# Kernel tuning notes

Measured on AMD Instinct MI355X. Metric: run time of the kernel, lower is better.

Reference implementation:

```python
import jax, jax.numpy as jnp
import numpy as np

B, T, C, H = 2, 2048, 1024, 16
HD = C // H

def setup_inputs() -> dict:
    key = jax.random.key(0)
    ks = jax.random.split(key, 5)
    x = jax.random.normal(ks[0], (B, T, C), dtype=jnp.float32)
    # causal mask, broadcast over batch and heads
    mask = jnp.tril(jnp.ones((T, T), dtype=jnp.int32))[None, None]
    scale = 0.02
    qkv_w = jax.random.normal(ks[1], (3 * C, C), dtype=jnp.float32) * scale
    qkv_b = jax.random.normal(ks[2], (3 * C,), dtype=jnp.float32) * scale
    out_w = jax.random.normal(ks[3], (C, C), dtype=jnp.float32) * scale
    out_b = jax.random.normal(ks[4], (C,), dtype=jnp.float32) * scale
    return {"x": x, "mask": mask, "qkv_w": qkv_w, "qkv_b": qkv_b,
            "out_w": out_w, "out_b": out_b}

def reference(x, mask, qkv_w, qkv_b, out_w, out_b):
    b, t, c = x.shape
    # torch Linear: y = x @ W^T + b
    qkv = jnp.einsum('btc,oc->bto', x, qkv_w) + qkv_b  # [B,T,3C]
    q, k, v = jnp.split(qkv, 3, axis=-1)
    def heads(u):
        return u.reshape(b, t, H, HD).transpose(0, 2, 1, 3)  # [B,H,T,HD]
    q, k, v = heads(q), heads(k), heads(v)
    attn = jnp.einsum('bhqd,bhkd->bhqk', q, k) / jnp.sqrt(jnp.float32(HD))
    attn = jnp.where(mask == 0, jnp.float32(-jnp.inf), attn)
    attn = jax.nn.softmax(attn, axis=-1)
    out = jnp.einsum('bhqk,bhkd->bhqd', attn, v)
    out = out.transpose(0, 2, 1, 3).reshape(b, t, c)
    return jnp.einsum('btc,oc->bto', out, out_w) + out_b
```

## Files before the change

kernel.cpp:

```cpp
#include <hip/hip_runtime.h>
#include <hip/hip_bf16.h>
#include <math.h>

#define B_  2
#define T_  2048
#define C_  1024
#define H_  16
#define HD_ 64

typedef __attribute__((ext_vector_type(8))) short short8;
typedef __attribute__((ext_vector_type(4))) float floatx4;

__device__ __forceinline__ short f2bf(float f) {
    __hip_bfloat16 h = __float2bfloat16(f);
    return *reinterpret_cast<short*>(&h);
}

__device__ __forceinline__ float fexp2(float x) {
#if __has_builtin(__builtin_amdgcn_exp2f)
    return __builtin_amdgcn_exp2f(x);
#else
    return exp2f(x);
#endif
}

__device__ __forceinline__ unsigned pack2bf(float a, float b) {
    return __builtin_amdgcn_perm(__float_as_uint(b), __float_as_uint(a),
                                 0x07060302u);
}

__device__ __forceinline__ void gld16(const void* g, void* l) {
    __builtin_amdgcn_global_load_lds(
        (const __attribute__((address_space(1))) void*)g,
        (__attribute__((address_space(3))) void*)l, 16, 0, 0);
}

__global__ __launch_bounds__(256)
void cast3(const float* __restrict__ x, const float* __restrict__ w1,
           const float* __restrict__ w2, short* __restrict__ xo,
           short* __restrict__ w1o, short* __restrict__ w2o)
{
    int gid = blockIdx.x * 256 + threadIdx.x;
    const float* s; short* d; int off;
    if (gid < 524288)      { s = x;  d = xo;  off = gid; }
    else if (gid < 917504) { s = w1; d = w1o; off = gid - 524288; }
    else                   { s = w2; d = w2o; off = gid - 917504; }
    float4 a = ((const float4*)s)[(size_t)off * 2];
    float4 b = ((const float4*)s)[(size_t)off * 2 + 1];
    short8 v;
    v[0] = f2bf(a.x); v[1] = f2bf(a.y); v[2] = f2bf(a.z); v[3] = f2bf(a.w);
    v[4] = f2bf(b.x); v[5] = f2bf(b.y); v[6] = f2bf(b.z); v[7] = f2bf(b.w);
    *(short8*)(d + (size_t)off * 8) = v;
}

template<int MODE, int BM, int BN, int BK>
__global__ __launch_bounds__(256, 4)
void gemm_bf16(const short* __restrict__ A, const short* __restrict__ W,
               const float* __restrict__ bias, float* __restrict__ out,
               short* __restrict__ qb, short* __restrict__ kb,
               short* __restrict__ vt, int M, int N, int K)
{
    constexpr int MI  = BM / 32;
    constexpr int NJ  = BN / 32;
    constexpr int KS  = BK / 32;
    constexpr int CPR = BK / 8;
    constexpr int LC  = (CPR == 8) ? 3 : 4;
    constexpr int RPT = 256 / CPR;
    __shared__ __align__(16) short As[2][BM * BK];
    __shared__ __align__(16) short Bs[2][BN * BK];

    const int tid  = threadIdx.x;
    const int lane = tid & 63;
    const int w    = tid >> 6;
    const int m    = lane & 15, quad = lane >> 4;
    const int wrow = w >> 1, wcol = w & 1;
    const int nb = blockIdx.x, mb = blockIdx.y;

    const int g = (tid & (CPR - 1)) ^ ((tid >> LC) & (CPR - 1));
    const short* Ag = A + (size_t)(mb * BM + (tid >> LC)) * K + g * 8;
    const short* Wg = W + (size_t)(nb * BN + (tid >> LC)) * K + g * 8;

    int aoff[MI][KS], boff[NJ][KS];
#pragma unroll
    for (int i = 0; i < MI; i++) {
        int ar = wrow * (BM / 2) + i * 16 + m;
#pragma unroll
        for (int ks = 0; ks < KS; ks++)
            aoff[i][ks] = ar * BK + (((ks * 4 + quad) ^ (ar & (CPR - 1))) * 8);
    }
#pragma unroll
    for (int j = 0; j < NJ; j++) {
        int bc = wcol * (BN / 2) + j * 16 + m;
#pragma unroll
        for (int ks = 0; ks < KS; ks++)
            boff[j][ks] = bc * BK + (((ks * 4 + quad) ^ (bc & (CPR - 1))) * 8);
    }

    floatx4 acc[MI][NJ];
#pragma unroll
    for (int i = 0; i < MI; i++)
#pragma unroll
        for (int j = 0; j < NJ; j++) acc[i][j] = (floatx4){0.f, 0.f, 0.f, 0.f};

    auto stage = [&](int k0, int bi) {
#pragma unroll
        for (int i = 0; i < BM / RPT; i++)
            gld16(Ag + (size_t)(i * RPT) * K + k0, As[bi] + i * 2048 + tid * 8);
#pragma unroll
        for (int i = 0; i < BN / RPT; i++)
            gld16(Wg + (size_t)(i * RPT) * K + k0, Bs[bi] + i * 2048 + tid * 8);
    };

    const int nk = K / BK;
    stage(0, 0);
    __syncthreads();

    for (int ki = 0; ki < nk; ki++) {
        const int cur = ki & 1;
        if (ki + 1 < nk) stage((ki + 1) * BK, cur ^ 1);

        const short* Ac = &As[cur][0];
        const short* Bc = &Bs[cur][0];
        short8 af[MI][KS], bfr[NJ][KS];
#pragma unroll
        for (int i = 0; i < MI; i++)
#pragma unroll
            for (int ks = 0; ks < KS; ks++)
                af[i][ks] = *(const short8*)(Ac + aoff[i][ks]);
#pragma unroll
        for (int j = 0; j < NJ; j++)
#pragma unroll
            for (int ks = 0; ks < KS; ks++)
                bfr[j][ks] = *(const short8*)(Bc + boff[j][ks]);
#pragma unroll
        for (int i = 0; i < MI; i++)
#pragma unroll
            for (int j = 0; j < NJ; j++)
#pragma unroll
                for (int ks = 0; ks < KS; ks++)
                    acc[i][j] = __builtin_amdgcn_mfma_f32_16x16x32_bf16(
                        af[i][ks], bfr[j][ks], acc[i][j], 0, 0, 0);
        __syncthreads();
    }

    const int row0 = mb * BM + wrow * (BM / 2);
    const int col0 = nb * BN + wcol * (BN / 2);

    if (MODE == 0) {
#pragma unroll
        for (int j = 0; j < NJ; j++) {
            int n = col0 + j * 16 + m;
            float bn = bias[n];
#pragma unroll
            for (int i = 0; i < MI; i++) {
#pragma unroll
                for (int r = 0; r < 4; r++) {
                    int mm = row0 + i * 16 + quad * 4 + r;
                    out[(size_t)mm * N + n] = acc[i][j][r] + bn;
                }
            }
        }
    } else {
        const int sec = col0 >> 10;
        const int h   = (col0 >> 6) & 15;
        if (sec <= 1) {
            short* dst = sec ? kb : qb;
            const float sc = sec ? 1.0f : 0.18033688011112042f;
#pragma unroll
            for (int j = 0; j < NJ; j++) {
                int n = col0 + j * 16 + m;
                int d = n & 63;
                float bn = bias[n];
#pragma unroll
                for (int i = 0; i < MI; i++) {
                    int t0 = row0 + i * 16 + quad * 4;
                    int b  = t0 >> 11;
                    int t  = t0 & (T_ - 1);
#pragma unroll
                    for (int r = 0; r < 4; r++)
                        dst[((size_t)(b * H_ + h) * T_ + t + r) * HD_ + d] =
                            f2bf((acc[i][j][r] + bn) * sc);
                }
            }
        } else {
#pragma unroll
            for (int j = 0; j < NJ; j++) {
                int n = col0 + j * 16 + m;
                int d = n & 63;
                float bn = bias[n];
#pragma unroll
                for (int i = 0; i < MI; i++) {
                    int t0 = row0 + i * 16 + quad * 4;
                    int b  = t0 >> 11;
                    int t  = t0 & (T_ - 1);
                    ushort4 u;
                    u.x = (unsigned short)f2bf(acc[i][j][0] + bn);
                    u.y = (unsigned short)f2bf(acc[i][j][1] + bn);
                    u.z = (unsigned short)f2bf(acc[i][j][2] + bn);
                    u.w = (unsigned short)f2bf(acc[i][j][3] + bn);
                    *(ushort4*)(vt + ((size_t)(b * H_ + h) * HD_ + d) * T_ + t) = u;
                }
            }
        }
    }
}

__global__ __launch_bounds__(256, 4)
void attn_mfma(const short* __restrict__ qb, const short* __restrict__ kb,
               const short* __restrict__ vt, short* __restrict__ ao)
{
    __shared__ __align__(16) short Ks[2][64 * 64];
    __shared__ __align__(16) short Vs[2][64 * 64];
    __shared__ __align__(16) short Ps[4][16 * 64];

    const int tid  = threadIdx.x;
    const int w    = tid >> 6;
    const int lane = tid & 63;
    const int m    = lane & 15;
    const int quad = lane >> 4;

    const int bid = blockIdx.x;
    const int r   = bid >> 8;
    const int bh  = ((bid & 7) << 2) | ((bid >> 3) & 3);
    const int qs  = (bid >> 5) & 7;
    const int qt  = r * 8 + ((r & 1) ? (7 - qs) : qs);
    const int b   = bh >> 4, h = bh & 15;

    int off8[8];
#pragma unroll
    for (int ks = 0; ks < 2; ks++)
#pragma unroll
        for (int nt = 0; nt < 4; nt++)
            off8[ks * 4 + nt] = (nt * 16 + m) * 64 + (((quad + 4 * ks) ^ (m & 7)) * 8);

    short* PsW = &Ps[w][0];
    int pw[4], pr[2];
#pragma unroll
    for (int nt = 0; nt < 4; nt++)
        pw[nt] = m * 64 + (((2 * nt + (quad >> 1)) ^ (m & 7)) * 8) + (quad & 1) * 4;
#pragma unroll
    for (int ks = 0; ks < 2; ks++)
        pr[ks] = m * 64 + (((4 * ks + quad) ^ (m & 7)) * 8);

    const short* kbh = kb + (size_t)bh * T_ * HD_;
    const short* vbh = vt + (size_t)bh * HD_ * T_;

    const short* qrowp = qb + ((size_t)bh * T_ + qt * 64 + w * 16 + m) * HD_;
    short8 bq0 = *(const short8*)(qrowp + quad * 8);
    short8 bq1 = *(const short8*)(qrowp + quad * 8 + 32);

    auto stage = [&](int kt2, int bi) {
        const int kbase = kt2 * 64;
#pragma unroll
        for (int it = 0; it < 2; it++) {
            int ci = it * 256 + tid;
            int rr = ci >> 3, cp = ci & 7, c = cp ^ (rr & 7);
            gld16(kbh + ((size_t)(kbase + rr)) * HD_ + c * 8, Ks[bi] + ci * 8);
            gld16(vbh + (size_t)rr * T_ + kbase + c * 8, Vs[bi] + ci * 8);
        }
    };

    stage(0, 0);
    __syncthreads();
    if (qt >= 1) stage(1, 1);

    floatx4 o[4];
#pragma unroll
    for (int nt = 0; nt < 4; nt++) o[nt] = (floatx4){0.f, 0.f, 0.f, 0.f};
    float lr = 0.f;

    for (int kt = 0; kt <= qt; kt++) {
        const int cur = kt & 1;
        const short* Kc = Ks[cur];
        const short* Vc = Vs[cur];

        floatx4 s[4];
#pragma unroll
        for (int nt = 0; nt < 4; nt++) {
            short8 k0 = *(const short8*)(Kc + off8[nt]);
            short8 k1 = *(const short8*)(Kc + off8[4 + nt]);
            floatx4 c = {0.f, 0.f, 0.f, 0.f};
            c = __builtin_amdgcn_mfma_f32_16x16x32_bf16(k0, bq0, c, 0, 0, 0);
            c = __builtin_amdgcn_mfma_f32_16x16x32_bf16(k1, bq1, c, 0, 0, 0);
            s[nt] = c;
        }

        if (kt == qt) {
#pragma unroll
            for (int nt = 0; nt < 4; nt++)
#pragma unroll
                for (int rr = 0; rr < 4; rr++)
                    if (nt * 16 + quad * 4 + rr > w * 16 + m) s[nt][rr] = -1e30f;
        }

        float rs = 0.f;
#pragma unroll
        for (int nt = 0; nt < 4; nt++) {
#pragma unroll
            for (int rr = 0; rr < 4; rr++) {
                float p = fexp2(s[nt][rr]);
                rs += p;
                s[nt][rr] = p;
            }
            uint2 pk;
            pk.x = pack2bf(s[nt][0], s[nt][1]);
            pk.y = pack2bf(s[nt][2], s[nt][3]);
            *(uint2*)(PsW + pw[nt]) = pk;
        }
        rs += __shfl_xor(rs, 16, 64);
        rs += __shfl_xor(rs, 32, 64);
        lr += rs;

        short8 pf0 = *(const short8*)(PsW + pr[0]);
        short8 pf1 = *(const short8*)(PsW + pr[1]);

#pragma unroll
        for (int nt = 0; nt < 4; nt++) {
            short8 v0 = *(const short8*)(Vc + off8[nt]);
            short8 v1 = *(const short8*)(Vc + off8[4 + nt]);
            o[nt] = __builtin_amdgcn_mfma_f32_16x16x32_bf16(v0, pf0, o[nt], 0, 0, 0);
            o[nt] = __builtin_amdgcn_mfma_f32_16x16x32_bf16(v1, pf1, o[nt], 0, 0, 0);
        }

        __syncthreads();
        if (kt + 2 <= qt) stage(kt + 2, cur);
    }

    const float inv = 1.0f / lr;
    const int qrow = qt * 64 + w * 16 + m;
    short* dst = ao + ((size_t)b * T_ + qrow) * C_ + h * HD_;
#pragma unroll
    for (int nt = 0; nt < 4; nt++) {
        ushort4 u;
        u.x = (unsigned short)f2bf(o[nt][0] * inv);
        u.y = (unsigned short)f2bf(o[nt][1] * inv);
        u.z = (unsigned short)f2bf(o[nt][2] * inv);
        u.w = (unsigned short)f2bf(o[nt][3] * inv);
        *(ushort4*)(dst + nt * 16 + quad * 4) = u;
    }
}

extern "C" void kernel_launch(void* const* d_in, const int* in_sizes, int n_in,
                              void* d_out, int out_size, void* d_ws, size_t ws_size,
                              hipStream_t stream)
{
    const float* x     = (const float*)d_in[0];
    const float* qkv_w = (const float*)d_in[2];
    const float* qkv_b = (const float*)d_in[3];
    const float* out_w = (const float*)d_in[4];
    const float* out_b = (const float*)d_in[5];
    float* out = (float*)d_out;

    const size_t BTC = (size_t)B_ * T_ * C_;
    short* xb  = (short*)d_ws;
    short* w1b = xb  + BTC;
    short* w2b = w1b + 3 * (size_t)C_ * C_;
    short* qbw = w2b + (size_t)C_ * C_;
    short* kbw = qbw + BTC;
    short* vtw = kbw + BTC;
    short* aob = vtw + BTC;

    cast3<<<4096, 256, 0, stream>>>(x, qkv_w, out_w, xb, w1b, w2b);

    dim3 g1(3 * C_ / 64, B_ * T_ / 128);
    gemm_bf16<1, 128, 64, 64><<<g1, 256, 0, stream>>>(xb, w1b, qkv_b, nullptr,
                                                      qbw, kbw, vtw,
                                                      B_ * T_, 3 * C_, C_);

    attn_mfma<<<1024, 256, 0, stream>>>(qbw, kbw, vtw, aob);

    dim3 g3(C_ / 64, B_ * T_ / 128);
    gemm_bf16<0, 128, 64, 64><<<g3, 256, 0, stream>>>(aob, w2b, out_b, out,
                                                      nullptr, nullptr, nullptr,
                                                      B_ * T_, C_, C_);
}
```

Measured before the change: 180.1 us.

## Double query rows per attention block to reuse K/V tiles across two row groups

Each attention block now covers 128 query rows instead of 64, with each wave handling two 16-row groups. Every staged K/V tile and its LDS fragments now feed twice as many MFMAs, which halves global K/V traffic and staging syncs per query row. In exchange the grid halves to 512 blocks, the launch-bounds occupancy hint drops to 2, register and P-buffer use double, and causal load balance across CUs becomes coarser.

```diff
diff --git a/kernel.cpp b/kernel.cpp
--- a/kernel.cpp
+++ b/kernel.cpp
@@ -205,13 +205,13 @@
     }
 }
 
-__global__ __launch_bounds__(256, 4)
+__global__ __launch_bounds__(256, 2)
 void attn_mfma(const short* __restrict__ qb, const short* __restrict__ kb,
                const short* __restrict__ vt, short* __restrict__ ao)
 {
     __shared__ __align__(16) short Ks[2][64 * 64];
     __shared__ __align__(16) short Vs[2][64 * 64];
-    __shared__ __align__(16) short Ps[4][16 * 64];
+    __shared__ __align__(16) short Ps[8][16 * 64];
 
     const int tid  = threadIdx.x;
     const int w    = tid >> 6;
@@ -233,7 +233,8 @@
         for (int nt = 0; nt < 4; nt++)
             off8[ks * 4 + nt] = (nt * 16 + m) * 64 + (((quad + 4 * ks) ^ (m & 7)) * 8);
 
-    short* PsW = &Ps[w][0];
+    short* Ps0 = &Ps[w * 2 + 0][0];
+    short* Ps1 = &Ps[w * 2 + 1][0];
     int pw[4], pr[2];
 #pragma unroll
     for (int nt = 0; nt < 4; nt++)
@@ -245,9 +246,12 @@
     const short* kbh = kb + (size_t)bh * T_ * HD_;
     const short* vbh = vt + (size_t)bh * HD_ * T_;
 
-    const short* qrowp = qb + ((size_t)bh * T_ + qt * 64 + w * 16 + m) * HD_;
-    short8 bq0 = *(const short8*)(qrowp + quad * 8);
-    short8 bq1 = *(const short8*)(qrowp + quad * 8 + 32);
+    const short* qp0 = qb + ((size_t)bh * T_ + qt * 128 + w * 32 + m) * HD_;
+    const short* qp1 = qp0 + 16 * HD_;
+    short8 qa0 = *(const short8*)(qp0 + quad * 8);
+    short8 qa1 = *(const short8*)(qp0 + quad * 8 + 32);
+    short8 qc0 = *(const short8*)(qp1 + quad * 8);
+    short8 qc1 = *(const short8*)(qp1 + quad * 8 + 32);
 
     auto stage = [&](int kt2, int bi) {
         const int kbase = kt2 * 64;
@@ -260,83 +264,109 @@
         }
     };
 
+    const int NTL = 2 * qt + 2;
+
     stage(0, 0);
     __syncthreads();
-    if (qt >= 1) stage(1, 1);
-
-    floatx4 o[4];
-#pragma unroll
-    for (int nt = 0; nt < 4; nt++) o[nt] = (floatx4){0.f, 0.f, 0.f, 0.f};
-    float lr = 0.f;
-
-    for (int kt = 0; kt <= qt; kt++) {
+    stage(1, 1);
+
+    floatx4 o0[4], o1[4];
+#pragma unroll
+    for (int nt = 0; nt < 4; nt++) {
+        o0[nt] = (floatx4){0.f, 0.f, 0.f, 0.f};
+        o1[nt] = (floatx4){0.f, 0.f, 0.f, 0.f};
+    }
+    float lr0 = 0.f, lr1 = 0.f;
+
+    for (int kt = 0; kt < NTL; kt++) {
         const int cur = kt & 1;
         const short* Kc = Ks[cur];
         const short* Vc = Vs[cur];
 
-        floatx4 s[4];
+        short8 kf0[4], kf1[4];
 #pragma unroll
         for (int nt = 0; nt < 4; nt++) {
-            short8 k0 = *(const short8*)(Kc + off8[nt]);
-            short8 k1 = *(const short8*)(Kc + off8[4 + nt]);
-            floatx4 c = {0.f, 0.f, 0.f, 0.f};
-            c = __builtin_amdgcn_mfma_f32_16x16x32_bf16(k0, bq0, c, 0, 0, 0);
-            c = __builtin_amdgcn_mfma_f32_16x16x32_bf16(k1, bq1, c, 0, 0, 0);
-            s[nt] = c;
+            kf0[nt] = *(const short8*)(Kc + off8[nt]);
+            kf1[nt] = *(const short8*)(Kc + off8[4 + nt]);
         }
 
-        if (kt == qt) {
-#pragma unroll
-            for (int nt = 0; nt < 4; nt++)
-#pragma unroll
-                for (int rr = 0; rr < 4; rr++)
-                    if (nt * 16 + quad * 4 + rr > w * 16 + m) s[nt][rr] = -1e30f;
-        }
-
-        float rs = 0.f;
-#pragma unroll
-        for (int nt = 0; nt < 4; nt++) {
-#pragma unroll
-            for (int rr = 0; rr < 4; rr++) {
-                float p = fexp2(s[nt][rr]);
-                rs += p;
-                s[nt][rr] = p;
-            }
-            uint2 pk;
-            pk.x = pack2bf(s[nt][0], s[nt][1]);
-            pk.y = pack2bf(s[nt][2], s[nt][3]);
-            *(uint2*)(PsW + pw[nt]) = pk;
-        }
-        rs += __shfl_xor(rs, 16, 64);
-        rs += __shfl_xor(rs, 32, 64);
-        lr += rs;
-
-        short8 pf0 = *(const short8*)(PsW + pr[0]);
-        short8 pf1 = *(const short8*)(PsW + pr[1]);
+        const int koff = (kt - 2 * qt) * 64;
+
+        auto qk_sm = [&](short8 qA, short8 qB, short* PsS, int qloc, float& lr) {
+            floatx4 s[4];
+#pragma unroll
+            for (int nt = 0; nt < 4; nt++) {
+                floatx4 c = {0.f, 0.f, 0.f, 0.f};
+                c = __builtin_amdgcn_mfma_f32_16x16x32_bf16(kf0[nt], qA, c, 0, 0, 0);
+                c = __builtin_amdgcn_mfma_f32_16x16x32_bf16(kf1[nt], qB, c, 0, 0, 0);
+                s[nt] = c;
+            }
+            if (kt >= 2 * qt) {
+#pragma unroll
+                for (int nt = 0; nt < 4; nt++)
+#pragma unroll
+                    for (int rr = 0; rr < 4; rr++)
+                        if (koff + nt * 16 + quad * 4 + rr > qloc) s[nt][rr] = -1e30f;
+            }
+            float rs = 0.f;
+#pragma unroll
+            for (int nt = 0; nt < 4; nt++) {
+#pragma unroll
+                for (int rr = 0; rr < 4; rr++) {
+                    float p = fexp2(s[nt][rr]);
+                    rs += p;
+                    s[nt][rr] = p;
+                }
+                uint2 pk;
+                pk.x = pack2bf(s[nt][0], s[nt][1]);
+                pk.y = pack2bf(s[nt][2], s[nt][3]);
+                *(uint2*)(PsS + pw[nt]) = pk;
+            }
+            rs += __shfl_xor(rs, 16, 64);
+            rs += __shfl_xor(rs, 32, 64);
+            lr += rs;
+        };
+        qk_sm(qa0, qa1, Ps0, w * 32 + m,      lr0);
+        qk_sm(qc0, qc1, Ps1, w * 32 + 16 + m, lr1);
+
+        short8 p00 = *(const short8*)(Ps0 + pr[0]);
+        short8 p01 = *(const short8*)(Ps0 + pr[1]);
+        short8 p10 = *(const short8*)(Ps1 + pr[0]);
+        short8 p11 = *(const short8*)(Ps1 + pr[1]);
 
 #pragma unroll
         for (int nt = 0; nt < 4; nt++) {
             short8 v0 = *(const short8*)(Vc + off8[nt]);
             short8 v1 = *(const short8*)(Vc + off8[4 + nt]);
-            o[nt] = __builtin_amdgcn_mfma_f32_16x16x32_bf16(v0, pf0, o[nt], 0, 0, 0);
-            o[nt] = __builtin_amdgcn_mfma_f32_16x16x32_bf16(v1, pf1, o[nt], 0, 0, 0);
+            o0[nt] = __builtin_amdgcn_mfma_f32_16x16x32_bf16(v0, p00, o0[nt], 0, 0, 0);
+            o0[nt] = __builtin_amdgcn_mfma_f32_16x16x32_bf16(v1, p01, o0[nt], 0, 0, 0);
+            o1[nt] = __builtin_amdgcn_mfma_f32_16x16x32_bf16(v0, p10, o1[nt], 0, 0, 0);
+            o1[nt] = __builtin_amdgcn_mfma_f32_16x16x32_bf16(v1, p11, o1[nt], 0, 0, 0);
         }
 
         __syncthreads();
-        if (kt + 2 <= qt) stage(kt + 2, cur);
-    }
-
-    const float inv = 1.0f / lr;
-    const int qrow = qt * 64 + w * 16 + m;
-    short* dst = ao + ((size_t)b * T_ + qrow) * C_ + h * HD_;
+        if (kt + 2 < NTL) stage(kt + 2, cur);
+    }
+
+    const float inv0 = 1.0f / lr0;
+    const float inv1 = 1.0f / lr1;
+    const int q0 = qt * 128 + w * 32 + m;
+    short* dst0 = ao + ((size_t)b * T_ + q0) * C_ + h * HD_;
+    short* dst1 = dst0 + 16 * C_;
 #pragma unroll
     for (int nt = 0; nt < 4; nt++) {
         ushort4 u;
-        u.x = (unsigned short)f2bf(o[nt][0] * inv);
-        u.y = (unsigned short)f2bf(o[nt][1] * inv);
-        u.z = (unsigned short)f2bf(o[nt][2] * inv);
-        u.w = (unsigned short)f2bf(o[nt][3] * inv);
-        *(ushort4*)(dst + nt * 16 + quad * 4) = u;
+        u.x = (unsigned short)f2bf(o0[nt][0] * inv0);
+        u.y = (unsigned short)f2bf(o0[nt][1] * inv0);
+        u.z = (unsigned short)f2bf(o0[nt][2] * inv0);
+        u.w = (unsigned short)f2bf(o0[nt][3] * inv0);
+        *(ushort4*)(dst0 + nt * 16 + quad * 4) = u;
+        ushort4 u2;
+        u2.x = (unsigned short)f2bf(o1[nt][0] * inv1);
+        u2.y = (unsigned short)f2bf(o1[nt][1] * inv1);
+        u2.z = (unsigned short)f2bf(o1[nt][2] * inv1);
+        u2.w = (unsigned short)f2bf(o1[nt][3] * inv1);
+        *(ushort4*)(dst1 + nt * 16 + quad * 4) = u2;
     }
 }
 
@@ -367,7 +397,7 @@
                                                       qbw, kbw, vtw,
                                                       B_ * T_, 3 * C_, C_);
 
-    attn_mfma<<<1024, 256, 0, stream>>>(qbw, kbw, vtw, aob);
+    attn_mfma<<<512, 256, 0, stream>>>(qbw, kbw, vtw, aob);
 
     dim3 g3(C_ / 64, B_ * T_ / 128);
     gemm_bf16<0, 128, 64, 64><<<g3, 256, 0, stream>>>(aob, w2b, out_b, out,
```

Measured after the change: 185.5 us. 1.03x slower.
